# Optimization experiments

Measured on AMD Instinct MI355X. Metric: run time of the kernel, lower is better.

Reference implementation:

```python
import jax
jax.config.update("jax_enable_x64", True)
import jax.numpy as jnp
import numpy as np

N = 20000      # nodes per batched graph
E = 320000     # random edges (avg degree 16)
F = 128        # input node features
EMB = 128      # embedding_size
H = 3          # num_heads
G = 128        # graphs in batch (for AvgPooling)
NEG_SLOPE = 0.2  # DGL GATConv attention LeakyReLU slope


def setup_inputs():
    key = jax.random.key(0)
    ks = jax.random.split(key, 40)

    def rn(k, shape):
        return jax.random.normal(k, shape, jnp.float32) * 0.1

    inp = {}
    inp["featsA"] = jax.random.normal(ks[0], (N, F), jnp.float32)
    inp["featsB"] = jax.random.normal(ks[1], (N, F), jnp.float32)
    # edges: random + self-loops so every node has >=1 incoming edge
    for nm, ka, kb in (("A", ks[2], ks[3]), ("B", ks[4], ks[5])):
        src = jnp.concatenate([jax.random.randint(ka, (E,), 0, N, jnp.int32),
                               jnp.arange(N, dtype=jnp.int32)])
        dst = jnp.concatenate([jax.random.randint(kb, (E,), 0, N, jnp.int32),
                               jnp.arange(N, dtype=jnp.int32)])
        inp["src" + nm] = src
        inp["dst" + nm] = dst
        inp["gid" + nm] = ((jnp.arange(N) * G) // N).astype(jnp.int32)

    # per-branch parameters (two independent GATNet_1 branches)
    i = 6
    for nm in ("A", "B"):
        inp["W1" + nm] = rn(ks[i], (F, H * EMB)); i += 1      # gat1A fc
        inp["al1" + nm] = rn(ks[i], (H, EMB)); i += 1          # attn_l
        inp["ar1" + nm] = rn(ks[i], (H, EMB)); i += 1          # attn_r
        inp["b1" + nm] = rn(ks[i], (H * EMB,)); i += 1         # bias
        inp["Wn" + nm] = rn(ks[i], (EMB, H * EMB)); i += 1     # gatn fc
        inp["aln" + nm] = rn(ks[i], (H, EMB)); i += 1
        inp["arn" + nm] = rn(ks[i], (H, EMB)); i += 1
        inp["bn" + nm] = rn(ks[i], (H * EMB,)); i += 1
        inp["Wl" + nm] = rn(ks[i], (H * EMB, EMB)); i += 1     # linear1A
        inp["bl" + nm] = rn(ks[i], (EMB,)); i += 1
    inp["Wo"] = rn(ks[i], (2 * EMB, 1)); i += 1                # DoubleNet.output
    inp["bo"] = rn(ks[i], (1,))
    return inp


def gat_layer(feat, src, dst, W, al, ar, b):
    # DGL GATConv (eval mode: feat_drop/attn_drop are identity)
    n = feat.shape[0]
    z = (feat @ W).reshape(n, H, -1)                     # [N,H,D]
    el = (z * al[None]).sum(-1)                          # [N,H]
    er = (z * ar[None]).sum(-1)
    e = jax.nn.leaky_relu(el[src] + er[dst], NEG_SLOPE)  # [E,H]
    # edge softmax over incoming edges of each dst node
    m = jax.ops.segment_max(e, dst, num_segments=n)
    a = jnp.exp(e - m[dst])
    den = jax.ops.segment_sum(a, dst, num_segments=n)
    a = a / den[dst]
    out = jax.ops.segment_sum(a[:, :, None] * z[src], dst, num_segments=n)  # [N,H,D]
    return out + b.reshape(1, H, -1)


def branch(feat, src, dst, gid, W1, al1, ar1, b1, Wn, aln, arn, bn, Wl, bl):
    n = feat.shape[0]
    x = gat_layer(feat, src, dst, W1, al1, ar1, b1).reshape(n, -1)
    x = x @ Wl + bl
    for _ in range(2):  # two applications of the SAME gatn/linear1A weights
        x = gat_layer(x, src, dst, Wn, aln, arn, bn).reshape(n, -1)
        x = x @ Wl + bl
        # nn.LeakyReLU(True): negative_slope == 1.0 -> identity (faithful)
    s = jax.ops.segment_sum(x, gid, num_segments=G)
    cnt = jax.ops.segment_sum(jnp.ones((n,), x.dtype), gid, num_segments=G)
    return s / cnt[:, None]


def reference(featsA, featsB, srcA, dstA, gidA, srcB, dstB, gidB,
              W1A, al1A, ar1A, b1A, WnA, alnA, arnA, bnA, WlA, blA,
              W1B, al1B, ar1B, b1B, WnB, alnB, arnB, bnB, WlB, blB,
              Wo, bo):
    x = branch(featsA, srcA, dstA, gidA, W1A, al1A, ar1A, b1A,
               WnA, alnA, arnA, bnA, WlA, blA)
    y = branch(featsB, srcB, dstB, gidB, W1B, al1B, ar1B, b1B,
               WnB, alnB, arnB, bnB, WlB, blB)
    cat = jnp.concatenate([x, y], axis=1)                # [G, 2*EMB]
    z = cat @ Wo + bo
    return z.astype(jnp.float64)                         # .double()
```

## Files before the change

### kernel.cpp

```cpp
#include <hip/hip_runtime.h>
#include <hip/hip_bf16.h>
#include <math.h>

#define NN  20000
#define FF  128
#define EMB 128
#define HH  3
#define GG  128
#define HD  384
#define ELL 64

typedef __attribute__((ext_vector_type(8))) short short8;
typedef __attribute__((ext_vector_type(4))) float f32x4;

__device__ inline float bf2f(unsigned int u){
  union{unsigned int i; float f;} v; v.i = u<<16; return v.f;
}
__device__ inline unsigned short f2bf(float f){
  union{unsigned int i; float f;} v; v.f = f;
  unsigned r = v.i + 0x7FFFu + ((v.i>>16)&1u);
  return (unsigned short)(r>>16);
}

__global__ __launch_bounds__(256) void prep(
    const float* __restrict__ W1A, const float* __restrict__ al1A, const float* __restrict__ ar1A,
    const float* __restrict__ WnA, const float* __restrict__ alnA, const float* __restrict__ arnA,
    const float* __restrict__ W1B, const float* __restrict__ al1B, const float* __restrict__ ar1B,
    const float* __restrict__ WnB, const float* __restrict__ alnB, const float* __restrict__ arnB,
    const float* __restrict__ WlA, const float* __restrict__ blA,
    const float* __restrict__ WlB, const float* __restrict__ blB,
    const float* __restrict__ b1A, const float* __restrict__ bnA,
    const float* __restrict__ b1B, const float* __restrict__ bnB,
    unsigned short* __restrict__ MT, float* __restrict__ V, float* __restrict__ cbuf,
    const int* __restrict__ srcA, const int* __restrict__ dstA,
    const int* __restrict__ srcB, const int* __restrict__ dstB,
    int* __restrict__ cntA, int* __restrict__ cntB,
    int* __restrict__ slotA, int* __restrict__ slotB, int ne, int nbE){
  __shared__ float As[32][65];
  __shared__ float Bs[32][65];
  int bid = blockIdx.x;
  int wv = threadIdx.x >> 6, lane = threadIdx.x & 63;

  if (bid < 48){
    int mh = bid >> 2;
    int mat = mh / 3, h = mh - mat*3;
    int tile = bid & 3; int tp = (tile>>1)*64, tq = (tile&1)*64;
    const float* W  = (mat==0)?W1A:(mat==1)?WnA:(mat==2)?W1B:WnB;
    const float* Wl = (mat<2)? WlA : WlB;
    int tid = threadIdx.x;
    int tq4 = (tid&15)<<2, tp4 = (tid>>4)<<2;
    float acc[4][4] = {};
    for (int d0=0; d0<128; d0+=32){
      {
        int p = tid>>3, dd = (tid&7)<<2;
        float4 a0 = *(const float4*)&W[(size_t)(tp+p)*HD + h*128 + d0 + dd];
        float4 a1 = *(const float4*)&W[(size_t)(tp+p+32)*HD + h*128 + d0 + dd];
        As[dd+0][p]=a0.x; As[dd+1][p]=a0.y; As[dd+2][p]=a0.z; As[dd+3][p]=a0.w;
        As[dd+0][p+32]=a1.x; As[dd+1][p+32]=a1.y; As[dd+2][p+32]=a1.z; As[dd+3][p+32]=a1.w;
      }
      {
        int dd = tid>>4, q4 = (tid&15)<<2;
        float4 b0 = *(const float4*)&Wl[(size_t)(h*128+d0+dd)*128 + tq + q4];
        float4 b1 = *(const float4*)&Wl[(size_t)(h*128+d0+dd+16)*128 + tq + q4];
        Bs[dd][q4+0]=b0.x; Bs[dd][q4+1]=b0.y; Bs[dd][q4+2]=b0.z; Bs[dd][q4+3]=b0.w;
        Bs[dd+16][q4+0]=b1.x; Bs[dd+16][q4+1]=b1.y; Bs[dd+16][q4+2]=b1.z; Bs[dd+16][q4+3]=b1.w;
      }
      __syncthreads();
      #pragma unroll
      for (int k=0;k<32;k++){
        float a[4], bb[4];
        #pragma unroll
        for (int i=0;i<4;i++) a[i] = As[k][tp4+i];
        #pragma unroll
        for (int jq=0;jq<4;jq++) bb[jq] = Bs[k][tq4+jq];
        #pragma unroll
        for (int i=0;i<4;i++)
          #pragma unroll
          for (int jq=0;jq<4;jq++)
            acc[i][jq] += a[i]*bb[jq];
      }
      __syncthreads();
    }
    #pragma unroll
    for (int jq=0;jq<4;jq++)
      #pragma unroll
      for (int i=0;i<4;i++)
        MT[(size_t)mat*49152 + (size_t)(tq+tq4+jq)*HD + h*128 + tp+tp4+i] = f2bf(acc[i][jq]);
  } else if (bid < 816){
    int idx = (bid-48)*4 + wv;
    int mat = idx / 768; int rem = idx - mat*768;
    int j = rem >> 7, k = rem & 127;
    int h = (j >= 3) ? j-3 : j; bool isr = j >= 3;
    const float* W = (mat==0)?W1A:(mat==1)?WnA:(mat==2)?W1B:WnB;
    const float* a;
    if (mat==0)      a = isr?ar1A:al1A;
    else if (mat==1) a = isr?arnA:alnA;
    else if (mat==2) a = isr?ar1B:al1B;
    else             a = isr?arnB:alnB;
    float s = W[(size_t)k*HD + h*128 + lane]      * a[h*128 + lane]
            + W[(size_t)k*HD + h*128 + 64 + lane] * a[h*128 + 64 + lane];
    #pragma unroll
    for (int o=32;o;o>>=1) s += __shfl_xor(s,o);
    if (lane == 0) V[(size_t)mat*768 + j*128 + k] = s;
  } else if (bid < 944){
    int idx = (bid-816)*4 + wv;
    int mat = idx >> 7, q = idx & 127;
    const float* bvec = (mat==0)?b1A:(mat==1)?bnA:(mat==2)?b1B:bnB;
    const float* Wl = (mat<2)?WlA:WlB;
    const float* bl = (mat<2)?blA:blB;
    float s = 0.f;
    #pragma unroll
    for (int r=0;r<6;r++){
      int j = r*64 + lane;
      s += bvec[j]*Wl[(size_t)j*128 + q];
    }
    #pragma unroll
    for (int o=32;o;o>>=1) s += __shfl_xor(s,o);
    if (lane == 0) cbuf[mat*128 + q] = s + bl[q];
  } else {
    int bb = bid - 944; int isB = bb >= nbE;
    const int* src = isB ? srcB : srcA;
    const int* dst = isB ? dstB : dstA;
    int* cnt  = isB ? cntB : cntA;
    int* slot = isB ? slotB : slotA;
    int i = (isB ? bb-nbE : bb)*256 + threadIdx.x;
    if (i < ne){
      int d = dst[i];
      int p = atomicAdd(&cnt[d], 1);
      if (p < ELL) slot[d*ELL + p] = src[i];
    }
  }
}

__global__ __launch_bounds__(256) void conv_elr1(
    const float* __restrict__ fA, const float* __restrict__ fB,
    unsigned short* __restrict__ XA, unsigned short* __restrict__ XB,
    const float* __restrict__ V,
    float* __restrict__ el, float* __restrict__ er){
  int gn = blockIdx.x*4 + (threadIdx.x>>6);
  int lane = threadIdx.x & 63;
  int b = gn >= NN; int n = b ? gn - NN : gn;
  const float* feats = b ? fB : fA;
  unsigned short* X = b ? XB : XA;
  const float* Vb = V + (size_t)(b*2 + 0)*768;
  float2 xv = ((const float2*)feats)[(size_t)n*64 + lane];
  ((unsigned*)(X + (size_t)n*EMB))[lane] =
      (unsigned)f2bf(xv.x) | ((unsigned)f2bf(xv.y)<<16);
  float x0 = bf2f((unsigned)f2bf(xv.x)), x1 = bf2f((unsigned)f2bf(xv.y));
  int c0 = 2*lane;
  #pragma unroll
  for (int j=0;j<6;j++){
    float v = x0*Vb[j*128 + c0] + x1*Vb[j*128 + c0 + 1];
    #pragma unroll
    for (int o=32;o;o>>=1) v += __shfl_xor(v,o);
    if (lane == 0){
      if (j < 3) el[(size_t)gn*4 + j] = v;
      else       er[(size_t)gn*4 + (j-3)] = v;
    }
  }
}

__global__ __launch_bounds__(256) void layer_fused(
    const unsigned short* __restrict__ X0, const unsigned short* __restrict__ X1,
    const float* __restrict__ el, const float* __restrict__ er,
    const int* __restrict__ cntA, const int* __restrict__ cntB,
    const int* __restrict__ slotA, const int* __restrict__ slotB,
    const unsigned short* __restrict__ MT_A, const unsigned short* __restrict__ MT_B,
    const float* __restrict__ cb_A, const float* __restrict__ cb_B,
    const float* __restrict__ V, int vsel,
    float* __restrict__ elN, float* __restrict__ erN,
    unsigned short* __restrict__ Xo0, unsigned short* __restrict__ Xo1){
  __shared__ unsigned short Ul[16][392];
  __shared__ float part[4][16][6];
  int wv = threadIdx.x >> 6, lane = threadIdx.x & 63;
  int bid = blockIdx.x;
  int b = bid >= (NN/16);
  int base = (b ? bid - NN/16 : bid) * 16;
  const unsigned short* X = b ? X1 : X0;
  const int* cnt  = b ? cntB : cntA;
  const int* slot = b ? slotB : slotA;
  const float* elb = el + (size_t)b*NN*4;
  const float* erb = er + (size_t)b*NN*4;

  const unsigned* Xw = (const unsigned*)X;
  for (int i = 0; i < 4; i++){
    int nloc = wv*4 + i;
    int n = base + nloc;
    int deg = cnt[n]; if (deg > ELL) deg = ELL;
    float er0 = erb[(size_t)n*4+0], er1 = erb[(size_t)n*4+1], er2 = erb[(size_t)n*4+2];

    int s = 0;
    float e0 = -3e38f, e1 = -3e38f, e2 = -3e38f;
    if (lane < deg){
      s = slot[n*ELL + lane];
      float4 ev = *(const float4*)(elb + (size_t)s*4);
      float t0 = ev.x+er0; e0 = t0>0.f ? t0 : 0.2f*t0;
      float t1 = ev.y+er1; e1 = t1>0.f ? t1 : 0.2f*t1;
      float t2 = ev.z+er2; e2 = t2>0.f ? t2 : 0.2f*t2;
    }
    float m0 = e0, m1 = e1, m2 = e2;
    #pragma unroll
    for (int o=32;o;o>>=1){
      m0 = fmaxf(m0, __shfl_xor(m0,o));
      m1 = fmaxf(m1, __shfl_xor(m1,o));
      m2 = fmaxf(m2, __shfl_xor(m2,o));
    }
    float p0 = __expf(e0-m0), p1 = __expf(e1-m1), p2 = __expf(e2-m2);
    float d0 = p0, d1 = p1, d2 = p2;
    #pragma unroll
    for (int o=32;o;o>>=1){
      d0 += __shfl_xor(d0,o); d1 += __shfl_xor(d1,o); d2 += __shfl_xor(d2,o);
    }
    float a0 = p0/d0, a1 = p1/d1, a2 = p2/d2;
    int a0i = __float_as_int(a0), a1i = __float_as_int(a1), a2i = __float_as_int(a2);

    float ax0=0.f,ay0=0.f,ax1=0.f,ay1=0.f,ax2=0.f,ay2=0.f;
    int npad = (deg + 3) & ~3;
    for (int e = 0; e < npad; e += 4){
      #pragma unroll
      for (int u2 = 0; u2 < 4; u2++){
        int idx = e + u2;
        int sl = __builtin_amdgcn_readlane(s, idx);
        float w0 = __int_as_float(__builtin_amdgcn_readlane(a0i, idx));
        float w1 = __int_as_float(__builtin_amdgcn_readlane(a1i, idx));
        float w2 = __int_as_float(__builtin_amdgcn_readlane(a2i, idx));
        unsigned xu = Xw[(size_t)sl*64 + lane];
        float lo = __int_as_float(xu << 16);
        float hi = __int_as_float(xu & 0xffff0000u);
        ax0 += w0*lo; ay0 += w0*hi;
        ax1 += w1*lo; ay1 += w1*hi;
        ax2 += w2*lo; ay2 += w2*hi;
      }
    }
    unsigned* urow = (unsigned*)&Ul[nloc][0];
    urow[lane]      = (unsigned)f2bf(ax0) | ((unsigned)f2bf(ay0)<<16);
    urow[64+lane]   = (unsigned)f2bf(ax1) | ((unsigned)f2bf(ay1)<<16);
    urow[128+lane]  = (unsigned)f2bf(ax2) | ((unsigned)f2bf(ay2)<<16);
  }
  __syncthreads();

  int l16 = lane & 15, lq = lane >> 4;
  const unsigned short* MTb = b ? MT_B : MT_A;
  int col0 = wv*32 + l16;
  int col1 = col0 + 16;
  const unsigned short* bp0 = MTb + (size_t)col0*HD + lq*8;
  const unsigned short* bp1 = MTb + (size_t)col1*HD + lq*8;
  f32x4 acc0 = {0.f,0.f,0.f,0.f}, acc1 = {0.f,0.f,0.f,0.f};
  #pragma unroll
  for (int k0 = 0; k0 < HD; k0 += 32){
    short8 af = *(const short8*)&Ul[l16][k0 + lq*8];
    short8 b0 = *(const short8*)&bp0[k0];
    short8 b1 = *(const short8*)&bp1[k0];
    acc0 = __builtin_amdgcn_mfma_f32_16x16x32_bf16(af, b0, acc0, 0, 0, 0);
    acc1 = __builtin_amdgcn_mfma_f32_16x16x32_bf16(af, b1, acc1, 0, 0, 0);
  }

  const float* cbb = b ? cb_B : cb_A;
  unsigned short* Xout = b ? Xo1 : Xo0;
  float cv0 = cbb[col0], cv1 = cbb[col1];
  float vv0[6], vv1[6];
  if (vsel >= 0){
    const float* Vv = V + (size_t)(b*2 + vsel)*768;
    #pragma unroll
    for (int j=0;j<6;j++){ vv0[j] = Vv[j*128 + col0]; vv1[j] = Vv[j*128 + col1]; }
  }
  #pragma unroll
  for (int r = 0; r < 4; r++){
    int nloc = lq*4 + r;
    int n = base + nloc;
    float x0 = acc0[r] + cv0, x1 = acc1[r] + cv1;
    unsigned short xb0 = f2bf(x0), xb1 = f2bf(x1);
    Xout[(size_t)n*EMB + col0] = xb0;
    Xout[(size_t)n*EMB + col1] = xb1;
    if (vsel >= 0){
      float xr0 = bf2f(xb0), xr1 = bf2f(xb1);
      float p[6];
      #pragma unroll
      for (int j=0;j<6;j++) p[j] = xr0*vv0[j] + xr1*vv1[j];
      #pragma unroll
      for (int j=0;j<6;j++){
        #pragma unroll
        for (int o=1;o<16;o<<=1) p[j] += __shfl_xor(p[j], o);
      }
      if (l16 == 0){
        #pragma unroll
        for (int j=0;j<6;j++) part[wv][nloc][j] = p[j];
      }
    }
  }
  if (vsel >= 0){
    __syncthreads();
    int t = threadIdx.x;
    if (t < 96){
      int nloc = t / 6, j = t - (t/6)*6;
      float s2 = part[0][nloc][j] + part[1][nloc][j] + part[2][nloc][j] + part[3][nloc][j];
      size_t gn = (size_t)b*NN + base + nloc;
      if (j < 3) elN[gn*4 + j] = s2;
      else       erN[gn*4 + (j-3)] = s2;
    }
  }
}

__device__ inline int lbound(const int* __restrict__ a, int n, int v){
  int lo = 0, hi = n;
  while (lo < hi){ int mid = (lo+hi)>>1; if (a[mid] < v) lo = mid+1; else hi = mid; }
  return lo;
}

__global__ __launch_bounds__(512) void pool_kernel(
    const unsigned short* __restrict__ X0, const unsigned short* __restrict__ X1,
    const int* __restrict__ gidA, const int* __restrict__ gidB,
    float* __restrict__ ps){
  int bg = blockIdx.x;
  int b = bg >= GG; int g = b ? bg-GG : bg;
  const unsigned short* X = b ? X1 : X0;
  const int* gid = b ? gidB : gidA;
  int lo = lbound(gid, NN, g), hi = lbound(gid, NN, g+1);
  int t = threadIdx.x;
  int rl = t >> 6, c2 = t & 63;
  float ax = 0.f, ay = 0.f;
  for (int n = lo + rl; n < hi; n += 8){
    unsigned u = ((const unsigned*)(X + (size_t)n*EMB))[c2];
    ax += bf2f(u & 0xFFFFu); ay += bf2f(u >> 16);
  }
  __shared__ float sh[8][128];
  sh[rl][2*c2] = ax; sh[rl][2*c2+1] = ay;
  __syncthreads();
  if (t < 128){
    float s = 0.f;
    #pragma unroll
    for (int r=0;r<8;r++) s += sh[r][t];
    ps[(size_t)bg*EMB + t] = s / (float)(hi - lo);
  }
}

__global__ void final_kernel(const float* __restrict__ ps,
                             const float* __restrict__ Wo, const float* __restrict__ bo,
                             float* __restrict__ out){
  int g = blockIdx.x*4 + (threadIdx.x>>6);
  int lane = threadIdx.x & 63;
  if (g >= GG) return;
  float v = 0.f;
  #pragma unroll
  for (int r=0;r<4;r++){
    int k = r*64 + lane;
    float cv = (k < EMB) ? ps[(size_t)g*EMB + k]
                         : ps[(size_t)(GG + g)*EMB + (k-EMB)];
    v += cv * Wo[k];
  }
  #pragma unroll
  for (int o=32;o;o>>=1) v += __shfl_xor(v,o);
  if (lane == 0) out[g] = v + bo[0];
}

extern "C" void kernel_launch(void* const* d_in, const int* in_sizes, int n_in,
                              void* d_out, int out_size, void* d_ws, size_t ws_size,
                              hipStream_t stream){
  const float* featsA = (const float*)d_in[0];
  const float* featsB = (const float*)d_in[1];
  const int* srcA = (const int*)d_in[2];
  const int* dstA = (const int*)d_in[3];
  const int* gidA = (const int*)d_in[4];
  const int* srcB = (const int*)d_in[5];
  const int* dstB = (const int*)d_in[6];
  const int* gidB = (const int*)d_in[7];
  const int EE = in_sizes[2];
  const float* P[2][10];
  for (int b=0;b<2;b++)
    for (int j=0;j<10;j++)
      P[b][j] = (const float*)d_in[8 + b*10 + j];
  const float* Wo = (const float*)d_in[28];
  const float* bo = (const float*)d_in[29];
  float* out = (float*)d_out;

  char* ws = (char*)d_ws;
  size_t o = 0;
  auto alloc = [&](size_t bytes)->char*{
    char* p = ws + o; o += (bytes + 255) & ~(size_t)255; return p;
  };
  unsigned short* fbf[2] = {(unsigned short*)alloc((size_t)NN*FF*2),
                            (unsigned short*)alloc((size_t)NN*FF*2)};
  unsigned short* Xa[2] = {(unsigned short*)alloc((size_t)NN*EMB*2),
                           (unsigned short*)alloc((size_t)NN*EMB*2)};
  unsigned short* Xb[2] = {(unsigned short*)alloc((size_t)NN*EMB*2),
                           (unsigned short*)alloc((size_t)NN*EMB*2)};
  unsigned short* MT = (unsigned short*)alloc((size_t)4*49152*2);
  float* V    = (float*)alloc((size_t)4*768*4);
  float* cbuf = (float*)alloc((size_t)4*128*4);
  float* el0  = (float*)alloc((size_t)2*NN*4*4);
  float* er0  = (float*)alloc((size_t)2*NN*4*4);
  float* el1  = (float*)alloc((size_t)2*NN*4*4);
  float* er1  = (float*)alloc((size_t)2*NN*4*4);
  float* el2  = (float*)alloc((size_t)2*NN*4*4);
  float* er2  = (float*)alloc((size_t)2*NN*4*4);
  int*   cntA = (int*)alloc((size_t)2*NN*4);
  int*   cntB = cntA + NN;
  int*   slotA= (int*)alloc((size_t)NN*ELL*4);
  int*   slotB= (int*)alloc((size_t)NN*ELL*4);
  float* ps   = (float*)alloc((size_t)2*GG*EMB*4);

  const int nbE = (EE + 255)/256;
  const int nwB = 2*NN/4;
  const int nLB = 2*NN/16;

  hipMemsetAsync(cntA, 0, (size_t)2*NN*4, stream);
  prep<<<944 + 2*nbE, 256, 0, stream>>>(
      P[0][0],P[0][1],P[0][2], P[0][4],P[0][5],P[0][6],
      P[1][0],P[1][1],P[1][2], P[1][4],P[1][5],P[1][6],
      P[0][8],P[0][9], P[1][8],P[1][9],
      P[0][3],P[0][7], P[1][3],P[1][7],
      MT, V, cbuf,
      srcA,dstA, srcB,dstB, cntA,cntB, slotA,slotB, EE, nbE);
  conv_elr1<<<nwB,256,0,stream>>>(featsA, featsB, fbf[0], fbf[1], V, el0, er0);

  layer_fused<<<nLB,256,0,stream>>>(fbf[0], fbf[1], el0, er0, cntA,cntB, slotA,slotB,
                                    MT + 0*49152, MT + 2*49152,
                                    cbuf + 0*128, cbuf + 2*128,
                                    V, 1, el1, er1, Xa[0], Xa[1]);
  layer_fused<<<nLB,256,0,stream>>>(Xa[0], Xa[1], el1, er1, cntA,cntB, slotA,slotB,
                                    MT + 1*49152, MT + 3*49152,
                                    cbuf + 1*128, cbuf + 3*128,
                                    V, 1, el2, er2, Xb[0], Xb[1]);
  layer_fused<<<nLB,256,0,stream>>>(Xb[0], Xb[1], el2, er2, cntA,cntB, slotA,slotB,
                                    MT + 1*49152, MT + 3*49152,
                                    cbuf + 1*128, cbuf + 3*128,
                                    V, -1, nullptr, nullptr, Xa[0], Xa[1]);

  pool_kernel<<<2*GG,512,0,stream>>>(Xa[0],Xa[1], gidA,gidB, ps);
  final_kernel<<<(GG+3)/4,256,0,stream>>>(ps, Wo, bo, out);
}
```

Measured before the change: 268.1 us.

## Interleave four nodes' edge gathers per wave and stage attention in LDS

```diff
diff --git a/kernel.cpp b/kernel.cpp
--- a/kernel.cpp
+++ b/kernel.cpp
@@ -170,72 +170,99 @@
     const float* __restrict__ V, int vsel,
     float* __restrict__ elN, float* __restrict__ erN,
     unsigned short* __restrict__ Xo0, unsigned short* __restrict__ Xo1){
+  __shared__ float4 ec[4][4][ELL];
   __shared__ unsigned short Ul[16][392];
   __shared__ float part[4][16][6];
   int wv = threadIdx.x >> 6, lane = threadIdx.x & 63;
   int bid = blockIdx.x;
-  int b = bid >= (NN/16);
-  int base = (b ? bid - NN/16 : bid) * 16;
+  int b = bid & 1;
+  int base = (bid >> 1) * 16;
   const unsigned short* X = b ? X1 : X0;
   const int* cnt  = b ? cntB : cntA;
   const int* slot = b ? slotB : slotA;
   const float* elb = el + (size_t)b*NN*4;
   const float* erb = er + (size_t)b*NN*4;
-
   const unsigned* Xw = (const unsigned*)X;
-  for (int i = 0; i < 4; i++){
-    int nloc = wv*4 + i;
-    int n = base + nloc;
-    int deg = cnt[n]; if (deg > ELL) deg = ELL;
-    float er0 = erb[(size_t)n*4+0], er1 = erb[(size_t)n*4+1], er2 = erb[(size_t)n*4+2];
-
+
+  int deg_[4]; int s_[4];
+  float e_[4][3];
+  #pragma unroll
+  for (int i=0;i<4;i++){
+    int n = base + wv*4 + i;
+    int dg = cnt[n]; if (dg > ELL) dg = ELL;
+    deg_[i] = dg;
+    float4 ev4 = *(const float4*)(erb + (size_t)n*4);
     int s = 0;
-    float e0 = -3e38f, e1 = -3e38f, e2 = -3e38f;
-    if (lane < deg){
+    float e0=-3e38f, e1=-3e38f, e2=-3e38f;
+    if (lane < dg){
       s = slot[n*ELL + lane];
-      float4 ev = *(const float4*)(elb + (size_t)s*4);
-      float t0 = ev.x+er0; e0 = t0>0.f ? t0 : 0.2f*t0;
-      float t1 = ev.y+er1; e1 = t1>0.f ? t1 : 0.2f*t1;
-      float t2 = ev.z+er2; e2 = t2>0.f ? t2 : 0.2f*t2;
-    }
-    float m0 = e0, m1 = e1, m2 = e2;
-    #pragma unroll
-    for (int o=32;o;o>>=1){
-      m0 = fmaxf(m0, __shfl_xor(m0,o));
-      m1 = fmaxf(m1, __shfl_xor(m1,o));
-      m2 = fmaxf(m2, __shfl_xor(m2,o));
-    }
-    float p0 = __expf(e0-m0), p1 = __expf(e1-m1), p2 = __expf(e2-m2);
-    float d0 = p0, d1 = p1, d2 = p2;
-    #pragma unroll
-    for (int o=32;o;o>>=1){
-      d0 += __shfl_xor(d0,o); d1 += __shfl_xor(d1,o); d2 += __shfl_xor(d2,o);
-    }
-    float a0 = p0/d0, a1 = p1/d1, a2 = p2/d2;
-    int a0i = __float_as_int(a0), a1i = __float_as_int(a1), a2i = __float_as_int(a2);
-
-    float ax0=0.f,ay0=0.f,ax1=0.f,ay1=0.f,ax2=0.f,ay2=0.f;
-    int npad = (deg + 3) & ~3;
-    for (int e = 0; e < npad; e += 4){
-      #pragma unroll
-      for (int u2 = 0; u2 < 4; u2++){
-        int idx = e + u2;
-        int sl = __builtin_amdgcn_readlane(s, idx);
-        float w0 = __int_as_float(__builtin_amdgcn_readlane(a0i, idx));
-        float w1 = __int_as_float(__builtin_amdgcn_readlane(a1i, idx));
-        float w2 = __int_as_float(__builtin_amdgcn_readlane(a2i, idx));
-        unsigned xu = Xw[(size_t)sl*64 + lane];
-        float lo = __int_as_float(xu << 16);
-        float hi = __int_as_float(xu & 0xffff0000u);
-        ax0 += w0*lo; ay0 += w0*hi;
-        ax1 += w1*lo; ay1 += w1*hi;
-        ax2 += w2*lo; ay2 += w2*hi;
-      }
-    }
-    unsigned* urow = (unsigned*)&Ul[nloc][0];
-    urow[lane]      = (unsigned)f2bf(ax0) | ((unsigned)f2bf(ay0)<<16);
-    urow[64+lane]   = (unsigned)f2bf(ax1) | ((unsigned)f2bf(ay1)<<16);
-    urow[128+lane]  = (unsigned)f2bf(ax2) | ((unsigned)f2bf(ay2)<<16);
+      float4 lv = *(const float4*)(elb + (size_t)s*4);
+      float t0 = lv.x+ev4.x; e0 = t0>0.f ? t0 : 0.2f*t0;
+      float t1 = lv.y+ev4.y; e1 = t1>0.f ? t1 : 0.2f*t1;
+      float t2 = lv.z+ev4.z; e2 = t2>0.f ? t2 : 0.2f*t2;
+    }
+    s_[i] = s; e_[i][0]=e0; e_[i][1]=e1; e_[i][2]=e2;
+  }
+  float m_[4][3];
+  #pragma unroll
+  for (int i=0;i<4;i++)
+    #pragma unroll
+    for (int h=0;h<3;h++) m_[i][h] = e_[i][h];
+  #pragma unroll
+  for (int o=32;o;o>>=1)
+    #pragma unroll
+    for (int i=0;i<4;i++)
+      #pragma unroll
+      for (int h=0;h<3;h++) m_[i][h] = fmaxf(m_[i][h], __shfl_xor(m_[i][h],o));
+  float p_[4][3], d_[4][3];
+  #pragma unroll
+  for (int i=0;i<4;i++)
+    #pragma unroll
+    for (int h=0;h<3;h++){ p_[i][h] = __expf(e_[i][h]-m_[i][h]); d_[i][h] = p_[i][h]; }
+  #pragma unroll
+  for (int o=32;o;o>>=1)
+    #pragma unroll
+    for (int i=0;i<4;i++)
+      #pragma unroll
+      for (int h=0;h<3;h++) d_[i][h] += __shfl_xor(d_[i][h],o);
+  #pragma unroll
+  for (int i=0;i<4;i++){
+    float4 t;
+    t.x = p_[i][0]/d_[i][0];
+    t.y = p_[i][1]/d_[i][1];
+    t.z = p_[i][2]/d_[i][2];
+    t.w = __int_as_float(s_[i]);
+    ec[wv][i][lane] = t;
+  }
+
+  int degmax = max(max(deg_[0],deg_[1]), max(deg_[2],deg_[3]));
+  float acc_[4][6] = {};
+  float4 tc[4];
+  #pragma unroll
+  for (int i=0;i<4;i++) tc[i] = ec[wv][i][0];
+  for (int e=0; e<degmax; e++){
+    int en = (e+1 < degmax) ? e+1 : e;
+    float4 tn[4];
+    #pragma unroll
+    for (int i=0;i<4;i++) tn[i] = ec[wv][i][en];
+    #pragma unroll
+    for (int i=0;i<4;i++){
+      unsigned xu = Xw[(size_t)__float_as_int(tc[i].w)*64 + lane];
+      float lo = __int_as_float(xu << 16);
+      float hi = __int_as_float(xu & 0xffff0000u);
+      acc_[i][0] += tc[i].x*lo; acc_[i][1] += tc[i].x*hi;
+      acc_[i][2] += tc[i].y*lo; acc_[i][3] += tc[i].y*hi;
+      acc_[i][4] += tc[i].z*lo; acc_[i][5] += tc[i].z*hi;
+    }
+    #pragma unroll
+    for (int i=0;i<4;i++) tc[i] = tn[i];
+  }
+  #pragma unroll
+  for (int i=0;i<4;i++){
+    unsigned* urow = (unsigned*)&Ul[wv*4 + i][0];
+    urow[lane]     = (unsigned)f2bf(acc_[i][0]) | ((unsigned)f2bf(acc_[i][1])<<16);
+    urow[64+lane]  = (unsigned)f2bf(acc_[i][2]) | ((unsigned)f2bf(acc_[i][3])<<16);
+    urow[128+lane] = (unsigned)f2bf(acc_[i][4]) | ((unsigned)f2bf(acc_[i][5])<<16);
   }
   __syncthreads();
 
```

Result: slower. 288.8 us (+7.7%).
